# Performance work log

Measured on AMD Instinct MI355X. Metric: run time of the kernel, lower is better.

Reference implementation:

```python
import jax, jax.numpy as jnp
import numpy as np

BS = 4  # gating blocksize


def setup_inputs() -> dict:
    key = jax.random.key(0)
    k1, k2, k3 = jax.random.split(key, 3)
    batch, rows, width, cols = 8, 2048, 4096, 4096
    X = jax.random.normal(k1, (batch, rows, width), dtype=jnp.float32)
    W = jax.random.normal(k2, (width, cols), dtype=jnp.float32)
    G = jax.random.normal(k3, (batch, width // BS, cols // BS), dtype=jnp.float32)
    return {"X": X, "W": W, "G": G}


def _gmm(X, W, G):
    # Y[b,r,c] = sum_k X[b,r,k] * W[k,c] * G[b, k//BS, c//BS]
    b = X.shape[0]
    # expand block gates to elementwise resolution
    Gf = jnp.repeat(jnp.repeat(G, BS, axis=1), BS, axis=2)  # (b, width, cols)
    # per-batch gated weight, then batched GEMM
    return jnp.einsum('brk,kc,bkc->brc', X, W, Gf)


def reference(X, W, G):
    Y = _gmm(X, W, G)
    s = Y.sum()
    return s * s
```

## Files before the change

### kernel.cpp

```cpp
#include <hip/hip_runtime.h>

#define BATCH 8
#define ROWS  2048
#define WIDTH 4096
#define COLS  4096
#define KB    1024
#define CB    1024
#define RCH   64

__global__ __launch_bounds__(256) void fused_kernel(const float4* __restrict__ Xv,
                                                    const float4* __restrict__ Wv,
                                                    const float* __restrict__ G,
                                                    float* __restrict__ xs,
                                                    float* __restrict__ wg) {
    const int tid = threadIdx.x;
    if (blockIdx.x & 1) {
        const int kb = blockIdx.x >> 1;
        float acc[8][4];
#pragma unroll
        for (int b = 0; b < 8; ++b)
#pragma unroll
            for (int j = 0; j < 4; ++j) acc[b][j] = 0.f;

#pragma unroll
        for (int chunk = 0; chunk < CB / 256; ++chunk) {
            const int cb = chunk * 256 + tid;
            float w4[4];
#pragma unroll
            for (int j = 0; j < 4; ++j) {
                float4 w = Wv[(size_t)(4 * kb + j) * CB + cb];
                w4[j] = (w.x + w.y) + (w.z + w.w);
            }
#pragma unroll
            for (int b = 0; b < 8; ++b) {
                float g = G[((size_t)b * KB + kb) * CB + cb];
#pragma unroll
                for (int j = 0; j < 4; ++j) acc[b][j] += g * w4[j];
            }
        }

        __shared__ float lds[4][32];
        const int lane = tid & 63, wid = tid >> 6;
#pragma unroll
        for (int v = 0; v < 32; ++v) {
            float x = acc[v >> 2][v & 3];
#pragma unroll
            for (int o = 1; o < 64; o <<= 1) x += __shfl_xor(x, o, 64);
            if (lane == 0) lds[wid][v] = x;
        }
        __syncthreads();
        if (tid < 32) {
            float r = lds[0][tid] + lds[1][tid] + lds[2][tid] + lds[3][tid];
            const int b = tid >> 2, j = tid & 3;
            wg[(size_t)b * WIDTH + 4 * kb + j] = r;
        }
    } else {
        const int c  = blockIdx.x >> 1;
        const int k4 = (c & 3) * 256 + tid;
        const int b  = (c >> 2) & 7;
        const int r0 = (c >> 5) * RCH;

        const float4* p = Xv + (size_t)(b * ROWS + r0) * (WIDTH / 4) + k4;
        float ax = 0.f, ay = 0.f, az = 0.f, aw = 0.f;
#pragma unroll 8
        for (int r = 0; r < RCH; ++r) {
            float4 v = p[(size_t)r * (WIDTH / 4)];
            ax += v.x; ay += v.y; az += v.z; aw += v.w;
        }
        float* dst = xs + (size_t)b * WIDTH + 4 * k4;
        atomicAdd(dst + 0, ax);
        atomicAdd(dst + 1, ay);
        atomicAdd(dst + 2, az);
        atomicAdd(dst + 3, aw);
    }
}

__global__ __launch_bounds__(256) void final_kernel(const float4* __restrict__ xs4,
                                                    const float4* __restrict__ wg4,
                                                    float* __restrict__ out) {
    float acc = 0.f;
    for (int i = threadIdx.x; i < BATCH * WIDTH / 4; i += 256) {
        float4 a = xs4[i], b = wg4[i];
        acc += a.x * b.x + a.y * b.y + a.z * b.z + a.w * b.w;
    }
    __shared__ float red[256];
    red[threadIdx.x] = acc;
    __syncthreads();
    for (int o = 128; o > 0; o >>= 1) {
        if (threadIdx.x < o) red[threadIdx.x] += red[threadIdx.x + o];
        __syncthreads();
    }
    if (threadIdx.x == 0) {
        float s = red[0];
        out[0] = s * s;
    }
}

extern "C" void kernel_launch(void* const* d_in, const int* in_sizes, int n_in,
                              void* d_out, int out_size, void* d_ws, size_t ws_size,
                              hipStream_t stream) {
    const float* X = (const float*)d_in[0];
    const float* W = (const float*)d_in[1];
    const float* G = (const float*)d_in[2];
    float* out = (float*)d_out;

    float* xs = (float*)d_ws;
    float* wg = xs + BATCH * WIDTH;

    hipMemsetAsync(xs, 0, (size_t)BATCH * WIDTH * sizeof(float), stream);

    fused_kernel<<<2048, 256, 0, stream>>>((const float4*)X, (const float4*)W, G, xs, wg);

    final_kernel<<<1, 256, 0, stream>>>((const float4*)xs, (const float4*)wg, out);
}
```

Measured before the change: 90.79 us.

## Rebalance X column-sum blocks into full-row slabs and widen final reduction

The X column-sum work is reorganised so each block sums a 32-row slab over the full 4096-wide row using four float4 accumulators per thread, instead of 64-row, 1024-column chunks. That gives 512 column-sum blocks instead of 1024, placed before the W/G blocks in the grid rather than interleaved. The final dot-product kernel now uses 1024 threads with a fully unrolled loop. The aim is better per-thread memory-level parallelism and fewer blocks, at the cost of more atomics per block and a different block scheduling order.

```diff
diff --git a/kernel.cpp b/kernel.cpp
--- a/kernel.cpp
+++ b/kernel.cpp
@@ -6,7 +6,9 @@
 #define COLS  4096
 #define KB    1024
 #define CB    1024
-#define RCH   64
+
+#define NCOLSUM 512
+#define SLABROWS 32
 
 __global__ __launch_bounds__(256) void fused_kernel(const float4* __restrict__ Xv,
                                                     const float4* __restrict__ Wv,
@@ -14,8 +16,44 @@
                                                     float* __restrict__ xs,
                                                     float* __restrict__ wg) {
     const int tid = threadIdx.x;
-    if (blockIdx.x & 1) {
-        const int kb = blockIdx.x >> 1;
+    if (blockIdx.x < NCOLSUM) {
+        const int s  = blockIdx.x;
+        const int b  = s >> 6;
+        const int r0 = (s & 63) * SLABROWS;
+        const float4* p = Xv + (size_t)(b * ROWS + r0) * (WIDTH / 4) + tid;
+
+        float4 a0 = {0, 0, 0, 0}, a1 = {0, 0, 0, 0}, a2 = {0, 0, 0, 0}, a3 = {0, 0, 0, 0};
+#pragma unroll 2
+        for (int ii = 0; ii < SLABROWS; ++ii) {
+            const float4* row = p + (size_t)ii * (WIDTH / 4);
+            float4 v0 = row[0];
+            float4 v1 = row[256];
+            float4 v2 = row[512];
+            float4 v3 = row[768];
+            a0.x += v0.x; a0.y += v0.y; a0.z += v0.z; a0.w += v0.w;
+            a1.x += v1.x; a1.y += v1.y; a1.z += v1.z; a1.w += v1.w;
+            a2.x += v2.x; a2.y += v2.y; a2.z += v2.z; a2.w += v2.w;
+            a3.x += v3.x; a3.y += v3.y; a3.z += v3.z; a3.w += v3.w;
+        }
+        float* dst = xs + (size_t)b * WIDTH;
+        atomicAdd(dst + 4 * (0 * 256 + tid) + 0, a0.x);
+        atomicAdd(dst + 4 * (0 * 256 + tid) + 1, a0.y);
+        atomicAdd(dst + 4 * (0 * 256 + tid) + 2, a0.z);
+        atomicAdd(dst + 4 * (0 * 256 + tid) + 3, a0.w);
+        atomicAdd(dst + 4 * (1 * 256 + tid) + 0, a1.x);
+        atomicAdd(dst + 4 * (1 * 256 + tid) + 1, a1.y);
+        atomicAdd(dst + 4 * (1 * 256 + tid) + 2, a1.z);
+        atomicAdd(dst + 4 * (1 * 256 + tid) + 3, a1.w);
+        atomicAdd(dst + 4 * (2 * 256 + tid) + 0, a2.x);
+        atomicAdd(dst + 4 * (2 * 256 + tid) + 1, a2.y);
+        atomicAdd(dst + 4 * (2 * 256 + tid) + 2, a2.z);
+        atomicAdd(dst + 4 * (2 * 256 + tid) + 3, a2.w);
+        atomicAdd(dst + 4 * (3 * 256 + tid) + 0, a3.x);
+        atomicAdd(dst + 4 * (3 * 256 + tid) + 1, a3.y);
+        atomicAdd(dst + 4 * (3 * 256 + tid) + 2, a3.z);
+        atomicAdd(dst + 4 * (3 * 256 + tid) + 3, a3.w);
+    } else {
+        const int kb = blockIdx.x - NCOLSUM;
         float acc[8][4];
 #pragma unroll
         for (int b = 0; b < 8; ++b)
@@ -54,39 +92,23 @@
             const int b = tid >> 2, j = tid & 3;
             wg[(size_t)b * WIDTH + 4 * kb + j] = r;
         }
-    } else {
-        const int c  = blockIdx.x >> 1;
-        const int k4 = (c & 3) * 256 + tid;
-        const int b  = (c >> 2) & 7;
-        const int r0 = (c >> 5) * RCH;
-
-        const float4* p = Xv + (size_t)(b * ROWS + r0) * (WIDTH / 4) + k4;
-        float ax = 0.f, ay = 0.f, az = 0.f, aw = 0.f;
-#pragma unroll 8
-        for (int r = 0; r < RCH; ++r) {
-            float4 v = p[(size_t)r * (WIDTH / 4)];
-            ax += v.x; ay += v.y; az += v.z; aw += v.w;
-        }
-        float* dst = xs + (size_t)b * WIDTH + 4 * k4;
-        atomicAdd(dst + 0, ax);
-        atomicAdd(dst + 1, ay);
-        atomicAdd(dst + 2, az);
-        atomicAdd(dst + 3, aw);
     }
 }
 
-__global__ __launch_bounds__(256) void final_kernel(const float4* __restrict__ xs4,
-                                                    const float4* __restrict__ wg4,
-                                                    float* __restrict__ out) {
+__global__ __launch_bounds__(1024) void final_kernel(const float4* __restrict__ xs4,
+                                                     const float4* __restrict__ wg4,
+                                                     float* __restrict__ out) {
     float acc = 0.f;
-    for (int i = threadIdx.x; i < BATCH * WIDTH / 4; i += 256) {
+#pragma unroll
+    for (int rep = 0; rep < BATCH * WIDTH / 4 / 1024; ++rep) {
+        int i = rep * 1024 + threadIdx.x;
         float4 a = xs4[i], b = wg4[i];
         acc += a.x * b.x + a.y * b.y + a.z * b.z + a.w * b.w;
     }
-    __shared__ float red[256];
+    __shared__ float red[1024];
     red[threadIdx.x] = acc;
     __syncthreads();
-    for (int o = 128; o > 0; o >>= 1) {
+    for (int o = 512; o > 0; o >>= 1) {
         if (threadIdx.x < o) red[threadIdx.x] += red[threadIdx.x + o];
         __syncthreads();
     }
@@ -109,7 +131,7 @@
 
     hipMemsetAsync(xs, 0, (size_t)BATCH * WIDTH * sizeof(float), stream);
 
-    fused_kernel<<<2048, 256, 0, stream>>>((const float4*)X, (const float4*)W, G, xs, wg);
+    fused_kernel<<<NCOLSUM + KB, 256, 0, stream>>>((const float4*)X, (const float4*)W, G, xs, wg);
 
-    final_kernel<<<1, 256, 0, stream>>>((const float4*)xs, (const float4*)wg, out);
+    final_kernel<<<1, 1024, 0, stream>>>((const float4*)xs, (const float4*)wg, out);
 }
```

Measured after the change: 99.02 us. 1.09x slower.
